# Kernel tuning notes

Measured on AMD Instinct MI355X. Metric: run time of the kernel, lower is better.

## Reference

```python
import jax, jax.numpy as jnp
import numpy as np

N_NODES = 100000
N_EDGES = 2000000
IN_C = 30
OUT_C = 10
HID = 4 * OUT_C      # 40
D1 = 2 * OUT_C       # 20
D2 = OUT_C           # 10
N_CLASSES = 3
K_SAMPLE = 8


def setup_inputs() -> dict:
    key = jax.random.key(0)
    ks = jax.random.split(key, 24)
    inp = {
        'x': jax.random.normal(ks[0], (N_NODES, IN_C), dtype=jnp.float32),
        'edge_index': jax.random.randint(ks[1], (2, N_EDGES), 0, N_NODES, dtype=jnp.int64),
        'edge_attr': jax.random.uniform(ks[2], (N_EDGES,), dtype=jnp.float32),
        'label': 1,
        # gcn1
        'W1': jax.random.normal(ks[3], (IN_C, HID), dtype=jnp.float32) * (1.0 / np.sqrt(IN_C)),
        'b1': jnp.zeros((HID,), jnp.float32),
        'ln1_w': jnp.ones((HID,), jnp.float32),
        'ln1_b': jnp.zeros((HID,), jnp.float32),
        # gcn2
        'W2': jax.random.normal(ks[4], (HID, HID), dtype=jnp.float32) * (1.0 / np.sqrt(HID)),
        'b2': jnp.zeros((HID,), jnp.float32),
        'ln2_w': jnp.ones((HID,), jnp.float32),
        'ln2_b': jnp.zeros((HID,), jnp.float32),
        # fnn
        'Wf': jax.random.normal(ks[5], (HID, D1), dtype=jnp.float32) * (1.0 / np.sqrt(HID)),
        'bf': jnp.zeros((D1,), jnp.float32),
        # attention (tanh / sigmoid branches + concat)
        'Wt': jax.random.normal(ks[6], (D1, D2), dtype=jnp.float32) * (1.0 / np.sqrt(D1)),
        'bt': jnp.zeros((D2,), jnp.float32),
        'Ws': jax.random.normal(ks[7], (D1, D2), dtype=jnp.float32) * (1.0 / np.sqrt(D1)),
        'bs': jnp.zeros((D2,), jnp.float32),
        'Wc': jax.random.normal(ks[8], (D2, 1), dtype=jnp.float32) * (1.0 / np.sqrt(D2)),
        'bc': jnp.zeros((1,), jnp.float32),
        # bag classifier
        'Wcls': jax.random.normal(ks[9], (D1, N_CLASSES), dtype=jnp.float32) * (1.0 / np.sqrt(D1)),
        'bcls': jnp.zeros((N_CLASSES,), jnp.float32),
        # per-class cell-scale classifiers, stacked [n_classes, D1, 2]
        'Wcell': jax.random.normal(ks[10], (N_CLASSES, D1, 2), dtype=jnp.float32) * (1.0 / np.sqrt(D1)),
        'bcell': jnp.zeros((N_CLASSES, 2), jnp.float32),
    }
    return inp


def _layernorm(x, w, b, eps=1e-5):
    m = jnp.mean(x, axis=-1, keepdims=True)
    v = jnp.var(x, axis=-1, keepdims=True)
    return (x - m) * jax.lax.rsqrt(v + eps) * w + b


def _gcn(x, W, b, src, dst, ew, n):
    # PyG GCNConv: add self-loops (weight 1), symmetric norm, aggregate at dst
    h = x @ W                                              # [N, F]
    deg = jax.ops.segment_sum(ew, dst, num_segments=n) + 1.0
    dinv = jnp.where(deg > 0, jax.lax.rsqrt(deg), 0.0)     # [N]
    norm = dinv[src] * ew * dinv[dst]                      # [E]
    agg = jax.ops.segment_sum(h[src] * norm[:, None], dst, num_segments=n)
    agg = agg + h * (dinv * dinv)[:, None]                 # self-loop term
    return agg + b


def _forward(x, edge_attr, W1, b1, ln1_w, ln1_b, W2, b2, ln2_w, ln2_b,
             Wf, bf, Wt, bt, Ws, bs, Wc, bc, Wcls, bcls, Wcell, bcell,
             edge_index, label):
    src, dst = edge_index[0], edge_index[1]
    n = x.shape[0]
    x1 = jax.nn.selu(_layernorm(_gcn(x, W1, b1, src, dst, edge_attr, n), ln1_w, ln1_b))
    x2 = jax.nn.selu(_layernorm(_gcn(x1, W2, b2, src, dst, edge_attr, n), ln2_w, ln2_b))
    x3 = jax.nn.selu(x2 @ Wf + bf)                         # [N, D1] == x_out
    # gated tanh*sigmoid attention
    gate = jnp.tanh(x3 @ Wt + bt) * jax.nn.sigmoid(x3 @ Ws + bs)
    A = (gate @ Wc + bc).T                                 # [1, N]
    A = jax.nn.softmax(A, axis=1)
    # cell-scale eval for the true class (one-hot label selects exactly one)
    a_row = A[-1]                                          # [N]
    _, idx_p = jax.lax.top_k(a_row, K_SAMPLE)
    _, idx_n = jax.lax.top_k(-a_row, K_SAMPLE)
    all_cells = jnp.concatenate([x3[idx_p], x3[idx_n]], axis=0)   # [2K, D1]
    logits_c = all_cells @ Wcell[label] + bcell[label]            # [2K, 2]
    targets = jnp.concatenate([jnp.ones((K_SAMPLE,), jnp.int32),
                               jnp.zeros((K_SAMPLE,), jnp.int32)])
    # SmoothTop1SVM (tau=1, alpha=1): mean( logsumexp(s + Delta) - s_y )
    delta = 1.0 - jax.nn.one_hot(targets, 2, dtype=logits_c.dtype)
    s_y = jnp.take_along_axis(logits_c, targets[:, None], axis=1)[:, 0]
    cell_loss = jnp.mean(jax.nn.logsumexp(logits_c + delta, axis=1) - s_y)
    # bag-level prediction
    x_pooled = A @ x3                                      # [1, D1]
    logits = x_pooled @ Wcls + bcls                        # [1, n_classes]
    Y_prob = jax.nn.softmax(logits, axis=1)
    Y_hat = jnp.argmax(logits, axis=1)[:, None]
    return logits, Y_prob, Y_hat, A, x3, cell_loss


def reference(x, edge_index, edge_attr, label, W1, b1, ln1_w, ln1_b, W2, b2,
              ln2_w, ln2_b, Wf, bf, Wt, bt, Ws, bs, Wc, bc, Wcls, bcls,
              Wcell, bcell):
    return _forward(x, edge_attr, W1, b1, ln1_w, ln1_b, W2, b2, ln2_w, ln2_b,
                    Wf, bf, Wt, bt, Ws, bs, Wc, bc, Wcls, bcls, Wcell, bcell,
                    edge_index, label)
```

## Files before the change

kernel.cpp:

```cpp
#include <hip/hip_runtime.h>
#include <hip/hip_bf16.h>
#include <math.h>

typedef __hip_bfloat16 bf16;

__device__ __forceinline__ float tof(bf16 v){ return __bfloat162float(v); }
__device__ __forceinline__ bf16  tob(float v){ return __float2bfloat16(v); }

__device__ __forceinline__ float sane(float v){
  return (v == v && v > -1e30f && v < 1e30f) ? v : 0.f;
}
__device__ __forceinline__ float ldf(const void* p, size_t i, bool f32){
  float v = f32 ? ((const float*)p)[i] : tof(((const bf16*)p)[i]);
  return sane(v);
}
__device__ __forceinline__ void stf(void* p, size_t i, float v, bool f32){
  if (f32) ((float*)p)[i] = v; else ((bf16*)p)[i] = tob(v);
}
__device__ __forceinline__ bool is_f32(const unsigned* __restrict__ dt){
  return dt[0] == 0x3F800000u;
}
__device__ __forceinline__ int clampi(int v, int hi){
  return ((unsigned)v < (unsigned)hi) ? v : 0;
}
__device__ __forceinline__ float selu_f(float x){
  const float sc = 1.0507009873554805f, al = 1.6732632423543772f;
  return x > 0.f ? sc * x : sc * al * (expf(x) - 1.0f);
}
__device__ __forceinline__ void unpack8(uint4 u, float* f){
  f[0]=__uint_as_float(u.x<<16); f[1]=__uint_as_float(u.x&0xFFFF0000u);
  f[2]=__uint_as_float(u.y<<16); f[3]=__uint_as_float(u.y&0xFFFF0000u);
  f[4]=__uint_as_float(u.z<<16); f[5]=__uint_as_float(u.z&0xFFFF0000u);
  f[6]=__uint_as_float(u.w<<16); f[7]=__uint_as_float(u.w&0xFFFF0000u);
}
__device__ __forceinline__ void unpack4(uint2 u, float* f){
  f[0]=__uint_as_float(u.x<<16); f[1]=__uint_as_float(u.x&0xFFFF0000u);
  f[2]=__uint_as_float(u.y<<16); f[3]=__uint_as_float(u.y&0xFFFF0000u);
}
__device__ __forceinline__ unsigned pack2(float a, float b){
  unsigned short ua, ub;
  bf16 ta = tob(a), tb = tob(b);
  __builtin_memcpy(&ua, &ta, 2);
  __builtin_memcpy(&ub, &tb, 2);
  return (unsigned)ua | ((unsigned)ub << 16);
}

__global__ void k_zero(float* __restrict__ p, int n){
  int i = blockIdx.x * blockDim.x + threadIdx.x;
  int stride = gridDim.x * blockDim.x;
  for (; i < n; i += stride) p[i] = 0.f;
}

__device__ __forceinline__ bool idx_is64(const int* __restrict__ raw){
  return ((raw[1] | raw[3] | raw[5] | raw[7] | raw[9] | raw[11]) == 0);
}
__device__ __forceinline__ void edge_at(const int* __restrict__ raw, int E, int e,
                                        bool w64, int N, int& s, int& d){
  int sv, dv;
  if (w64){ sv = raw[2 * e]; dv = raw[2 * (E + e)]; }
  else    { sv = raw[e];     dv = raw[E + e]; }
  s = clampi(sv, N); d = clampi(dv, N);
}

__global__ void k_cnt_rank(const int* __restrict__ raw, int* __restrict__ cnt,
                           int* __restrict__ rank, int E, int N){
  int e = blockIdx.x * blockDim.x + threadIdx.x;
  if (e >= E) return;
  bool w64 = idx_is64(raw);
  int s, d; edge_at(raw, E, e, w64, N, s, d);
  rank[e] = atomicAdd(&cnt[d], 1);
}

__global__ void k_scan_block(const int* __restrict__ cnt, int* __restrict__ bsum, int N){
  __shared__ int s[256];
  int base = blockIdx.x * 1024;
  int acc = 0;
  for (int k = threadIdx.x; k < 1024; k += 256){
    int i = base + k;
    acc += (i < N) ? cnt[i] : 0;
  }
  s[threadIdx.x] = acc; __syncthreads();
  for (int w = 128; w > 0; w >>= 1){
    if (threadIdx.x < w) s[threadIdx.x] += s[threadIdx.x + w];
    __syncthreads();
  }
  if (threadIdx.x == 0) bsum[blockIdx.x] = s[0];
}

__global__ void k_scan_partials(int* __restrict__ bsum, int B, int* __restrict__ rowpN, int E){
  __shared__ int s[256];
  int run = 0;
  for (int t0 = 0; t0 < B; t0 += 256){
    int i = t0 + threadIdx.x;
    int v = (i < B) ? bsum[i] : 0;
    s[threadIdx.x] = v;
    __syncthreads();
    for (int o = 1; o < 256; o <<= 1){
      int add = (threadIdx.x >= o) ? s[threadIdx.x - o] : 0;
      __syncthreads();
      s[threadIdx.x] += add;
      __syncthreads();
    }
    int incl = s[threadIdx.x];
    int total = s[255];
    __syncthreads();
    if (i < B) bsum[i] = run + incl - v;
    run += total;
    __syncthreads();
  }
  if (threadIdx.x == 0) rowpN[0] = E;
}

__global__ void k_scan_final(const int* __restrict__ cnt, const int* __restrict__ bsum,
                             int* __restrict__ rowp, int N){
  __shared__ int s[256];
  int t = threadIdx.x;
  int base = bsum[blockIdx.x];
  int i0 = blockIdx.x * 1024 + t * 4;
  int v0=0,v1=0,v2=0,v3=0;
  if (i0+0 < N) v0 = cnt[i0+0];
  if (i0+1 < N) v1 = cnt[i0+1];
  if (i0+2 < N) v2 = cnt[i0+2];
  if (i0+3 < N) v3 = cnt[i0+3];
  int sum = v0+v1+v2+v3;
  s[t] = sum; __syncthreads();
  for (int o = 1; o < 256; o <<= 1){
    int add = (t >= o) ? s[t - o] : 0;
    __syncthreads();
    s[t] += add;
    __syncthreads();
  }
  int off = base + s[t] - sum;
  if (i0+0 < N){ rowp[i0+0]=off; off+=v0; }
  if (i0+1 < N){ rowp[i0+1]=off; off+=v1; }
  if (i0+2 < N){ rowp[i0+2]=off; off+=v2; }
  if (i0+3 < N){ rowp[i0+3]=off; off+=v3; }
}

__global__ void k_place(const int* __restrict__ raw, const void* __restrict__ ea,
                        const unsigned* __restrict__ dt, const int* __restrict__ rank,
                        const int* __restrict__ rowp, int2* __restrict__ ep, int E, int N){
  int e = blockIdx.x * blockDim.x + threadIdx.x;
  if (e >= E) return;
  bool f32 = is_f32(dt);
  bool w64 = idx_is64(raw);
  int s, d; edge_at(raw, E, e, w64, N, s, d);
  float w = ldf(ea, e, f32);
  int pos = rowp[d] + rank[e];
  if ((unsigned)pos < (unsigned)E)
    ep[pos] = make_int2(s, __float_as_int(w));
}

__global__ void k_dinv_csr(const int* __restrict__ rowp, const int2* __restrict__ ep,
                           float* __restrict__ dinv, int N, int E){
  int n = blockIdx.x * blockDim.x + threadIdx.x;
  if (n >= N) return;
  int beg = rowp[n], end = rowp[n + 1];
  if (beg < 0) beg = 0;
  if (end > E) end = E;
  float s = 0.f;
  for (int j = beg; j < end; j++) s += sane(__int_as_float(ep[j].y));
  float dv = s + 1.0f;
  dinv[n] = (dv > 0.f) ? rsqrtf(dv) : 0.f;
}

__global__ void k_premul(int2* __restrict__ ep, const float* __restrict__ dinv,
                         int E, int N){
  int i = blockIdx.x * blockDim.x + threadIdx.x;
  if (i >= E) return;
  int2 p = ep[i];
  int s = clampi(p.x, N);
  float w = dinv[s] * sane(__int_as_float(p.y));
  ep[i] = make_int2(s, __float_as_int(w));
}

__global__ void k_mm1(const void* __restrict__ X, const void* __restrict__ W,
                      const unsigned* __restrict__ dt,
                      bf16* __restrict__ H, int N, int Nx){
  bool f32 = is_f32(dt);
  __shared__ float w[30 * 40];
  __shared__ float xs[256 * 30];
  for (int i = threadIdx.x; i < 30 * 40; i += 256) w[i] = ldf(W, i, f32);
  int base = blockIdx.x * 256;
  int rows = Nx - base; if (rows > 256) rows = 256; if (rows < 0) rows = 0;
  int nelem = rows * 30;
  size_t gbase = (size_t)base * 30;
  for (int i = threadIdx.x; i < nelem; i += 256) xs[i] = ldf(X, gbase + i, f32);
  __syncthreads();
  int n = base + threadIdx.x;
  if (n >= N) return;
  float acc[40];
  #pragma unroll
  for (int j = 0; j < 40; j++) acc[j] = 0.f;
  if (threadIdx.x < rows){
    const float* xr = &xs[threadIdx.x * 30];
    for (int i = 0; i < 30; i++){
      float xi = xr[i];
      #pragma unroll
      for (int j = 0; j < 40; j++) acc[j] += xi * w[i * 40 + j];
    }
  } else {
    for (int i = 0; i < 30; i++){
      float xi = ldf(X, i, f32);
      #pragma unroll
      for (int j = 0; j < 40; j++) acc[j] += xi * w[i * 40 + j];
    }
  }
  uint4 ob[5];
  unsigned* ou = (unsigned*)ob;
  #pragma unroll
  for (int q = 0; q < 20; q++) ou[q] = pack2(acc[2*q], acc[2*q+1]);
  uint4* op = (uint4*)(H + (size_t)n * 40);
  #pragma unroll
  for (int q = 0; q < 5; q++) op[q] = ob[q];
}

__global__ void k_mm2(const bf16* __restrict__ X, const void* __restrict__ W,
                      const unsigned* __restrict__ dt,
                      bf16* __restrict__ H, int N){
  bool f32 = is_f32(dt);
  __shared__ float w[40 * 40];
  for (int i = threadIdx.x; i < 40 * 40; i += 256) w[i] = ldf(W, i, f32);
  __syncthreads();
  int n = blockIdx.x * blockDim.x + threadIdx.x;
  if (n >= N) return;
  float acc[40];
  #pragma unroll
  for (int j = 0; j < 40; j++) acc[j] = 0.f;
  const uint4* xp = (const uint4*)(X + (size_t)n * 40);
  #pragma unroll
  for (int q = 0; q < 5; q++){
    uint4 u = xp[q];
    float f[8]; unpack8(u, f);
    #pragma unroll
    for (int k = 0; k < 8; k++){
      float xi = f[k];
      int i = q * 8 + k;
      #pragma unroll
      for (int j = 0; j < 40; j++) acc[j] += xi * w[i * 40 + j];
    }
  }
  uint4 ob[5];
  unsigned* ou = (unsigned*)ob;
  #pragma unroll
  for (int q = 0; q < 20; q++) ou[q] = pack2(acc[2*q], acc[2*q+1]);
  uint4* op = (uint4*)(H + (size_t)n * 40);
  #pragma unroll
  for (int q = 0; q < 5; q++) op[q] = ob[q];
}

__global__ void k_gather(const int* __restrict__ rowp, const int2* __restrict__ ep,
                         const bf16* __restrict__ h, const float* __restrict__ dinv,
                         const void* __restrict__ b, const void* __restrict__ lw,
                         const void* __restrict__ lb, const unsigned* __restrict__ dt,
                         bf16* __restrict__ xout, int N, int E){
  int n = (blockIdx.x * blockDim.x + threadIdx.x) >> 6;
  int lane = threadIdx.x & 63;
  if (n >= N) return;
  bool f32 = is_f32(dt);
  bool act = lane < 40;
  float dn = dinv[n];
  int beg = rowp[n], end = rowp[n + 1];
  if (beg < 0) beg = 0;
  if (end > E) end = E;
  float acc = 0.f;
  int j = beg;
  for (; j + 3 < end; j += 4){
    int2 p0 = ep[j+0], p1 = ep[j+1], p2 = ep[j+2], p3 = ep[j+3];
    int s0 = clampi(p0.x, N), s1 = clampi(p1.x, N);
    int s2 = clampi(p2.x, N), s3 = clampi(p3.x, N);
    float h0 = 0.f, h1 = 0.f, h2 = 0.f, h3 = 0.f;
    if (act){
      h0 = tof(h[(size_t)s0 * 40 + lane]);
      h1 = tof(h[(size_t)s1 * 40 + lane]);
      h2 = tof(h[(size_t)s2 * 40 + lane]);
      h3 = tof(h[(size_t)s3 * 40 + lane]);
    }
    acc += h0 * __int_as_float(p0.y) + h1 * __int_as_float(p1.y)
         + h2 * __int_as_float(p2.y) + h3 * __int_as_float(p3.y);
  }
  for (; j < end; j++){
    int2 p = ep[j];
    int s = clampi(p.x, N);
    float hv = act ? tof(h[(size_t)s * 40 + lane]) : 0.f;
    acc += hv * __int_as_float(p.y);
  }
  acc *= dn;
  float hself = act ? tof(h[(size_t)n * 40 + lane]) : 0.f;
  float v = act ? (sane(acc) + hself * dn * dn + ldf(b, lane, f32)) : 0.f;
  float sum = v;
  #pragma unroll
  for (int o = 1; o < 64; o <<= 1) sum += __shfl_xor(sum, o);
  float m = sum * (1.0f / 40.0f);
  float d = act ? (v - m) : 0.f;
  float sq = d * d;
  #pragma unroll
  for (int o = 1; o < 64; o <<= 1) sq += __shfl_xor(sq, o);
  float inv = rsqrtf(sq * (1.0f / 40.0f) + 1e-5f);
  if (act){
    float y = sane(selu_f(d * inv * ldf(lw, lane, f32) + ldf(lb, lane, f32)));
    xout[(size_t)n * 40 + lane] = tob(y);
  }
}

__global__ void k_head(const bf16* __restrict__ x2,
                       const void* __restrict__ Wf, const void* __restrict__ bfv,
                       const void* __restrict__ Wt, const void* __restrict__ bt,
                       const void* __restrict__ Ws, const void* __restrict__ bs,
                       const void* __restrict__ Wc, const void* __restrict__ bc,
                       const unsigned* __restrict__ dt,
                       bf16* __restrict__ x3ws, float* __restrict__ alog, int N){
  bool f32 = is_f32(dt);
  __shared__ float wf[800], bff[20], wt[200], btt[10], wss[200], bss[10], wc[10], bcc[1];
  for (int i = threadIdx.x; i < 800; i += blockDim.x) wf[i] = ldf(Wf, i, f32);
  for (int i = threadIdx.x; i < 200; i += blockDim.x){
    wt[i] = ldf(Wt, i, f32); wss[i] = ldf(Ws, i, f32);
  }
  if (threadIdx.x < 20) bff[threadIdx.x] = ldf(bfv, threadIdx.x, f32);
  if (threadIdx.x < 10){ btt[threadIdx.x] = ldf(bt, threadIdx.x, f32);
                         bss[threadIdx.x] = ldf(bs, threadIdx.x, f32);
                         wc[threadIdx.x]  = ldf(Wc, threadIdx.x, f32); }
  if (threadIdx.x == 0) bcc[0] = ldf(bc, 0, f32);
  __syncthreads();
  int n = blockIdx.x * blockDim.x + threadIdx.x;
  if (n >= N) return;
  float r[40];
  const uint4* xp = (const uint4*)(x2 + (size_t)n * 40);
  #pragma unroll
  for (int q = 0; q < 5; q++){
    uint4 u = xp[q];
    unpack8(u, &r[q * 8]);
  }
  float x3r[20];
  #pragma unroll
  for (int j = 0; j < 20; j++){
    float acc = bff[j];
    for (int i = 0; i < 40; i++) acc += r[i] * wf[i * 20 + j];
    x3r[j] = sane(selu_f(acc));
  }
  uint2 ob[5];
  unsigned* ou = (unsigned*)ob;
  #pragma unroll
  for (int q = 0; q < 10; q++) ou[q] = pack2(x3r[2*q], x3r[2*q+1]);
  uint2* op = (uint2*)(x3ws + (size_t)n * 20);
  #pragma unroll
  for (int q = 0; q < 5; q++) op[q] = ob[q];
  float a = bcc[0];
  #pragma unroll
  for (int j = 0; j < 10; j++){
    float zt = btt[j], zs = bss[j];
    for (int i = 0; i < 20; i++){ zt += x3r[i] * wt[i * 10 + j]; zs += x3r[i] * wss[i * 10 + j]; }
    float g = tanhf(zt) * (1.0f / (1.0f + expf(-zs)));
    a += g * wc[j];
  }
  alog[n] = sane(a);
}

__global__ void k_copy_x3(const bf16* __restrict__ x3ws, const unsigned* __restrict__ dt,
                          void* __restrict__ out, size_t off, int total){
  bool f32 = is_f32(dt);
  int i = blockIdx.x * blockDim.x + threadIdx.x;
  int stride = gridDim.x * blockDim.x;
  for (; i < total; i += stride) stf(out, off + i, tof(x3ws[i]), f32);
}

__global__ void k_msum(const float* __restrict__ a, float2* __restrict__ part, int n){
  __shared__ float sm[256], sl[256];
  int t = threadIdx.x;
  float m = -1e30f, l = 0.f;
  for (int i = blockIdx.x * blockDim.x + t; i < n; i += gridDim.x * blockDim.x){
    float v = sane(a[i]);
    if (v > m){ l = l * expf(m - v) + 1.f; m = v; }
    else        l += expf(v - m);
  }
  sm[t] = m; sl[t] = l; __syncthreads();
  for (int w = 128; w > 0; w >>= 1){
    if (t < w){
      float m2 = sm[t+w], l2 = sl[t+w];
      float mm = fmaxf(sm[t], m2);
      sl[t] = sl[t] * expf(sm[t] - mm) + l2 * expf(m2 - mm);
      sm[t] = mm;
    }
    __syncthreads();
  }
  if (t == 0) part[blockIdx.x] = make_float2(sm[0], sl[0]);
}

__global__ void k_msum_fin(const float2* __restrict__ part, float* __restrict__ scal,
                           float* __restrict__ pooled){
  __shared__ float sm[256], sl[256];
  int t = threadIdx.x;
  float2 p = part[t];
  sm[t] = p.x; sl[t] = p.y; __syncthreads();
  for (int w = 128; w > 0; w >>= 1){
    if (t < w){
      float m2 = sm[t+w], l2 = sl[t+w];
      float mm = fmaxf(sm[t], m2);
      sl[t] = sl[t] * expf(sm[t] - mm) + l2 * expf(m2 - mm);
      sm[t] = mm;
    }
    __syncthreads();
  }
  if (t == 0){ scal[0] = sm[0]; scal[1] = sl[0]; }
  if (t < 20) pooled[t] = 0.f;
}

__global__ void k_writeA(const float* __restrict__ alog, const bf16* __restrict__ x3ws,
                         const float* __restrict__ scal,
                         const unsigned* __restrict__ dt,
                         void* __restrict__ out, size_t a_off,
                         float* __restrict__ pooled, int N){
  bool f32 = is_f32(dt);
  float gmax = scal[0];
  float sum  = scal[1];
  float inv  = (sum > 0.f) ? 1.0f / sum : 0.f;
  float acc[20];
  #pragma unroll
  for (int j = 0; j < 20; j++) acc[j] = 0.f;
  for (int i = blockIdx.x * blockDim.x + threadIdx.x; i < N; i += gridDim.x * blockDim.x){
    float a = expf(sane(alog[i]) - gmax) * inv;
    stf(out, a_off + i, a, f32);
    const uint2* xr = (const uint2*)(x3ws + (size_t)i * 20);
    #pragma unroll
    for (int q = 0; q < 5; q++){
      float f[4]; unpack4(xr[q], f);
      #pragma unroll
      for (int k = 0; k < 4; k++) acc[q * 4 + k] += a * f[k];
    }
  }
  __shared__ float s[20];
  if (threadIdx.x < 20) s[threadIdx.x] = 0.f;
  __syncthreads();
  #pragma unroll
  for (int j = 0; j < 20; j++) atomicAdd(&s[j], acc[j]);
  __syncthreads();
  if (threadIdx.x < 20) atomicAdd(&pooled[threadIdx.x], s[threadIdx.x]);
}

__global__ void k_topk1(const float* __restrict__ a, int N,
                        float* __restrict__ cvp, int* __restrict__ cip,
                        float* __restrict__ cvn, int* __restrict__ cin){
  const int T = 256, K = 8;
  __shared__ float sv[T * K];
  __shared__ int   si[T * K];
  __shared__ float rv[T];
  __shared__ int   ri[T];
  __shared__ int   rs[T];
  int t = threadIdx.x;
  float tv[K]; int ti[K]; float bv[K]; int bi[K];
  #pragma unroll
  for (int k = 0; k < K; k++){ tv[k] = -1e38f; ti[k] = 0x7ffffff;
                               bv[k] =  1e38f; bi[k] = 0x7ffffff; }
  for (int i = blockIdx.x * T + t; i < N; i += gridDim.x * T){
    float v = sane(a[i]);
    if (v > tv[K-1]){
      int p = K - 1;
      while (p > 0 && v > tv[p-1]){ tv[p] = tv[p-1]; ti[p] = ti[p-1]; p--; }
      tv[p] = v; ti[p] = i;
    }
    if (v < bv[K-1]){
      int p = K - 1;
      while (p > 0 && v < bv[p-1]){ bv[p] = bv[p-1]; bi[p] = bi[p-1]; p--; }
      bv[p] = v; bi[p] = i;
    }
  }
  for (int k = 0; k < K; k++){ sv[t*K+k] = tv[k]; si[t*K+k] = ti[k]; }
  __syncthreads();
  for (int round = 0; round < K; round++){
    float bvv = -1e38f; int bii = 0x7ffffff; int bslot = 0;
    for (int k = 0; k < K; k++){
      float v = sv[t*K+k]; int ii = si[t*K+k];
      if (v > bvv || (v == bvv && ii < bii)){ bvv = v; bii = ii; bslot = t*K+k; }
    }
    rv[t] = bvv; ri[t] = bii; rs[t] = bslot;
    __syncthreads();
    for (int w = T/2; w > 0; w >>= 1){
      if (t < w){
        float v2 = rv[t+w]; int i2 = ri[t+w];
        if (v2 > rv[t] || (v2 == rv[t] && i2 < ri[t])){ rv[t]=v2; ri[t]=i2; rs[t]=rs[t+w]; }
      }
      __syncthreads();
    }
    if (t == 0){ cvp[blockIdx.x*K + round] = rv[0]; cip[blockIdx.x*K + round] = ri[0];
                 sv[rs[0]] = -1e38f; }
    __syncthreads();
  }
  for (int k = 0; k < K; k++){ sv[t*K+k] = bv[k]; si[t*K+k] = bi[k]; }
  __syncthreads();
  for (int round = 0; round < K; round++){
    float bvv = 1e38f; int bii = 0x7ffffff; int bslot = 0;
    for (int k = 0; k < K; k++){
      float v = sv[t*K+k]; int ii = si[t*K+k];
      if (v < bvv || (v == bvv && ii < bii)){ bvv = v; bii = ii; bslot = t*K+k; }
    }
    rv[t] = bvv; ri[t] = bii; rs[t] = bslot;
    __syncthreads();
    for (int w = T/2; w > 0; w >>= 1){
      if (t < w){
        float v2 = rv[t+w]; int i2 = ri[t+w];
        if (v2 < rv[t] || (v2 == rv[t] && i2 < ri[t])){ rv[t]=v2; ri[t]=i2; rs[t]=rs[t+w]; }
      }
      __syncthreads();
    }
    if (t == 0){ cvn[blockIdx.x*K + round] = rv[0]; cin[blockIdx.x*K + round] = ri[0];
                 sv[rs[0]] = 1e38f; }
    __syncthreads();
  }
}

__global__ void k_topk2(const float* __restrict__ cvp, const int* __restrict__ cip,
                        const float* __restrict__ cvn, const int* __restrict__ cin,
                        int* __restrict__ idxp, int* __restrict__ idxn, int M){
  const int T = 256, CAP = 1024, PER = CAP / T;
  __shared__ float sv[CAP];
  __shared__ int   si[CAP];
  __shared__ float rv[T];
  __shared__ int   ri[T];
  __shared__ int   rs[T];
  int t = threadIdx.x;
  for (int i = t; i < CAP; i += T){
    sv[i] = (i < M) ? cvp[i] : -1e38f;
    si[i] = (i < M) ? cip[i] : 0x7ffffff;
  }
  __syncthreads();
  for (int round = 0; round < 8; round++){
    float bvv = -1e38f; int bii = 0x7ffffff; int bslot = t * PER;
    for (int k = 0; k < PER; k++){
      float v = sv[t*PER+k]; int ii = si[t*PER+k];
      if (v > bvv || (v == bvv && ii < bii)){ bvv = v; bii = ii; bslot = t*PER+k; }
    }
    rv[t] = bvv; ri[t] = bii; rs[t] = bslot;
    __syncthreads();
    for (int w = T/2; w > 0; w >>= 1){
      if (t < w){
        float v2 = rv[t+w]; int i2 = ri[t+w];
        if (v2 > rv[t] || (v2 == rv[t] && i2 < ri[t])){ rv[t]=v2; ri[t]=i2; rs[t]=rs[t+w]; }
      }
      __syncthreads();
    }
    if (t == 0){ idxp[round] = ri[0]; sv[rs[0]] = -1e38f; }
    __syncthreads();
  }
  for (int i = t; i < CAP; i += T){
    sv[i] = (i < M) ? cvn[i] : 1e38f;
    si[i] = (i < M) ? cin[i] : 0x7ffffff;
  }
  __syncthreads();
  for (int round = 0; round < 8; round++){
    float bvv = 1e38f; int bii = 0x7ffffff; int bslot = t * PER;
    for (int k = 0; k < PER; k++){
      float v = sv[t*PER+k]; int ii = si[t*PER+k];
      if (v < bvv || (v == bvv && ii < bii)){ bvv = v; bii = ii; bslot = t*PER+k; }
    }
    rv[t] = bvv; ri[t] = bii; rs[t] = bslot;
    __syncthreads();
    for (int w = T/2; w > 0; w >>= 1){
      if (t < w){
        float v2 = rv[t+w]; int i2 = ri[t+w];
        if (v2 < rv[t] || (v2 == rv[t] && i2 < ri[t])){ rv[t]=v2; ri[t]=i2; rs[t]=rs[t+w]; }
      }
      __syncthreads();
    }
    if (t == 0){ idxn[round] = ri[0]; sv[rs[0]] = 1e38f; }
    __syncthreads();
  }
}

__global__ void k_final(const float* __restrict__ pooled,
                        const void* __restrict__ Wcls, const void* __restrict__ bcls,
                        const void* __restrict__ Wcell, const void* __restrict__ bcell,
                        const int* __restrict__ label_p, const bf16* __restrict__ x3ws,
                        const int* __restrict__ idxp, const int* __restrict__ idxn,
                        const unsigned* __restrict__ dt,
                        void* __restrict__ out, int N){
  if (threadIdx.x != 0 || blockIdx.x != 0) return;
  bool f32 = is_f32(dt);
  float lg[3];
  for (int c = 0; c < 3; c++){
    float acc = ldf(bcls, c, f32);
    for (int j = 0; j < 20; j++) acc += sane(pooled[j]) * ldf(Wcls, j * 3 + c, f32);
    lg[c] = sane(acc);
  }
  float m = fmaxf(lg[0], fmaxf(lg[1], lg[2]));
  float e0 = expf(lg[0]-m), e1 = expf(lg[1]-m), e2 = expf(lg[2]-m);
  float es = e0 + e1 + e2;
  int yhat = 0;
  if (lg[1] > lg[yhat]) yhat = 1;
  if (lg[2] > lg[yhat]) yhat = 2;
  stf(out, 0, lg[0], f32); stf(out, 1, lg[1], f32); stf(out, 2, lg[2], f32);
  stf(out, 3, e0/es, f32); stf(out, 4, e1/es, f32); stf(out, 5, e2/es, f32);
  stf(out, 6, (float)yhat, f32);
  int lw0 = label_p[0];
  int label;
  if ((unsigned)lw0 < 3u) label = lw0;
  else if (lw0 == 0x3F800000 || lw0 == 0x3F803F80) label = 1;
  else if (lw0 == 0x40000000 || lw0 == 0x40004000) label = 2;
  else label = 0;
  float w0[20], w1[20];
  for (int j = 0; j < 20; j++){
    w0[j] = ldf(Wcell, (size_t)label * 40 + j*2 + 0, f32);
    w1[j] = ldf(Wcell, (size_t)label * 40 + j*2 + 1, f32);
  }
  float b0 = ldf(bcell, (size_t)label * 2 + 0, f32);
  float b1 = ldf(bcell, (size_t)label * 2 + 1, f32);
  float loss = 0.f;
  for (int i = 0; i < 16; i++){
    int node = clampi((i < 8) ? idxp[i] : idxn[i-8], N);
    const bf16* xr = x3ws + (size_t)node * 20;
    float l0 = b0, l1 = b1;
    for (int j = 0; j < 20; j++){ float xv = tof(xr[j]); l0 += xv * w0[j]; l1 += xv * w1[j]; }
    int tgt = (i < 8) ? 1 : 0;
    float a0 = l0 + ((tgt == 0) ? 0.f : 1.f);
    float a1 = l1 + ((tgt == 1) ? 0.f : 1.f);
    float mm = fmaxf(a0, a1);
    float lse = mm + logf(expf(a0-mm) + expf(a1-mm));
    float sy = tgt ? l1 : l0;
    loss += lse - sy;
  }
  stf(out, (size_t)7 + N + (size_t)20 * N, sane(loss * (1.0f / 16.0f)), f32);
}

extern "C" void kernel_launch(void* const* d_in, const int* in_sizes, int n_in,
                              void* d_out, int out_size, void* d_ws, size_t ws_size,
                              hipStream_t stream) {
  const int N = (out_size - 8) / 21;
  if (N <= 0) return;
  const int Nx = (in_sizes[0] / 30 < N) ? (in_sizes[0] / 30) : N;
  int E = in_sizes[1] / 2;
  if (in_sizes[2] < E) E = in_sizes[2];
  if (E < 6) return;

  const void* x    = d_in[0];
  const int*  eraw = (const int*)d_in[1];
  const void* ea   = d_in[2];
  const int*  lbl  = (const int*)d_in[3];
  const void* W1   = d_in[4];
  const void* b1   = d_in[5];
  const unsigned* dt = (const unsigned*)d_in[6];
  const void* ln1w = d_in[6];
  const void* ln1b = d_in[7];
  const void* W2   = d_in[8];
  const void* b2   = d_in[9];
  const void* ln2w = d_in[10];
  const void* ln2b = d_in[11];
  const void* Wf   = d_in[12];
  const void* bfv  = d_in[13];
  const void* Wt   = d_in[14];
  const void* bt   = d_in[15];
  const void* Ws   = d_in[16];
  const void* bs   = d_in[17];
  const void* Wc   = d_in[18];
  const void* bc   = d_in[19];
  const void* Wcls = d_in[20];
  const void* bcls = d_in[21];
  const void* Wcell= d_in[22];
  const void* bcell= d_in[23];

  auto align16 = [](size_t v){ return (v + 15) & ~(size_t)15; };
  size_t hA_bytes = (size_t)N * 40 * 2;
  size_t rank_bytes = (size_t)E * 4;
  size_t regA = hA_bytes > rank_bytes ? hA_bytes : rank_bytes;
  size_t off = 0;
  char* ws = (char*)d_ws;
  bf16* hA    = (bf16*)(ws + off);
  int*  rank  = (int*)(ws + off);  off = align16(off + regA);
  bf16* xB    = (bf16*)(ws + off); off = align16(off + (size_t)N * 40 * 2);
  int2* epack = (int2*)(ws + off); off = align16(off + (size_t)E * 8);
  int*  rowp  = (int*)(ws + off);  off = align16(off + (size_t)(N + 1) * 4);
  int*  cnt   = (int*)(ws + off);  off = align16(off + (size_t)N * 4);
  int*  bsum  = (int*)(ws + off);  off = align16(off + 4096 * 4);
  float* dinv = (float*)(ws + off); off = align16(off + (size_t)N * 4);
  float* alog = (float*)(ws + off); off = align16(off + (size_t)N * 4);
  float2* part2 = (float2*)(ws + off); off = align16(off + 256 * 8);
  float* scal = (float*)(ws + off); off = align16(off + 2 * 4);
  float* pooled = (float*)(ws + off); off = align16(off + 20 * 4);
  int*   idxp = (int*)(ws + off); off = align16(off + 8 * 4);
  int*   idxn = (int*)(ws + off); off = align16(off + 8 * 4);
  float* cvp  = (float*)(ws + off); off = align16(off + 1024 * 4);
  int*   cip  = (int*)(ws + off);   off = align16(off + 1024 * 4);
  float* cvn  = (float*)(ws + off); off = align16(off + 1024 * 4);
  int*   cin  = (int*)(ws + off);   off = align16(off + 1024 * 4);
  if (off > ws_size) return;
  bf16* x3ws = hA;

  const int TB = 256;
  const int gN = (N + TB - 1) / TB;
  const int gE = (E + TB - 1) / TB;
  const int gW = (N + 3) / 4;
  const int SB = (N + 1023) / 1024;
  const int TP = 128;

  k_zero<<<gN, TB, 0, stream>>>((float*)cnt, N);
  k_cnt_rank<<<gE, TB, 0, stream>>>(eraw, cnt, rank, E, N);
  k_scan_block<<<SB, TB, 0, stream>>>(cnt, bsum, N);
  k_scan_partials<<<1, TB, 0, stream>>>(bsum, SB, rowp + N, E);
  k_scan_final<<<SB, TB, 0, stream>>>(cnt, bsum, rowp, N);
  k_place<<<gE, TB, 0, stream>>>(eraw, ea, dt, rank, rowp, epack, E, N);
  k_dinv_csr<<<gN, TB, 0, stream>>>(rowp, epack, dinv, N, E);
  k_premul<<<gE, TB, 0, stream>>>(epack, dinv, E, N);

  k_mm1<<<gN, TB, 0, stream>>>(x, W1, dt, hA, N, Nx);
  k_gather<<<gW, TB, 0, stream>>>(rowp, epack, hA, dinv, b1, ln1w, ln1b, dt, xB, N, E);

  k_mm2<<<gN, TB, 0, stream>>>(xB, W2, dt, hA, N);
  k_gather<<<gW, TB, 0, stream>>>(rowp, epack, hA, dinv, b2, ln2w, ln2b, dt, xB, N, E);

  k_head<<<gN, TB, 0, stream>>>(xB, Wf, bfv, Wt, bt, Ws, bs, Wc, bc, dt,
                                x3ws, alog, N);
  k_copy_x3<<<2048, TB, 0, stream>>>(x3ws, dt, d_out, (size_t)7 + N, 20 * N);

  k_msum<<<256, TB, 0, stream>>>(alog, part2, N);
  k_msum_fin<<<1, TB, 0, stream>>>(part2, scal, pooled);
  k_writeA<<<256, TB, 0, stream>>>(alog, x3ws, scal, dt, d_out, (size_t)7, pooled, N);

  k_topk1<<<TP, TB, 0, stream>>>(alog, N, cvp, cip, cvn, cin);
  k_topk2<<<1, TB, 0, stream>>>(cvp, cip, cvn, cin, idxp, idxn, TP * 8);
  k_final<<<1, 64, 0, stream>>>(pooled, Wcls, bcls, Wcell, bcell, lbl,
                                x3ws, idxp, idxn, dt, d_out, N);
}
```

Baseline: 681.2 us.

## Gather with 8 lanes per node and 16-byte vectorized feature loads

The GCN aggregation kernel used to give each node a full 64-lane wavefront, with only 40 lanes active and one bf16 loaded per lane. It now gives each node 8 lanes, 5 of them active, and each active lane loads 8 bf16 features as one uint4 per neighbour. LayerNorm reductions shrink to 3 shuffle steps, and the output is written with one vector store per lane. The aim is fewer idle lanes, fewer memory instructions and more nodes in flight per wave. The trade-off is more registers per thread and divergence when nodes in the same wave have very different degrees.

```diff
diff --git a/kernel.cpp b/kernel.cpp
--- a/kernel.cpp
+++ b/kernel.cpp
@@ -254,52 +254,84 @@
                          const void* __restrict__ b, const void* __restrict__ lw,
                          const void* __restrict__ lb, const unsigned* __restrict__ dt,
                          bf16* __restrict__ xout, int N, int E){
-  int n = (blockIdx.x * blockDim.x + threadIdx.x) >> 6;
-  int lane = threadIdx.x & 63;
+  int tid = blockIdx.x * blockDim.x + threadIdx.x;
+  int n  = tid >> 3;
+  int sl = tid & 7;
   if (n >= N) return;
   bool f32 = is_f32(dt);
-  bool act = lane < 40;
+  bool act = sl < 5;
+  int fb = sl * 8;
   float dn = dinv[n];
   int beg = rowp[n], end = rowp[n + 1];
   if (beg < 0) beg = 0;
   if (end > E) end = E;
-  float acc = 0.f;
+  float a[8];
+  #pragma unroll
+  for (int k = 0; k < 8; k++) a[k] = 0.f;
   int j = beg;
   for (; j + 3 < end; j += 4){
-    int2 p0 = ep[j+0], p1 = ep[j+1], p2 = ep[j+2], p3 = ep[j+3];
+    int2 p0 = ep[j], p1 = ep[j+1], p2 = ep[j+2], p3 = ep[j+3];
     int s0 = clampi(p0.x, N), s1 = clampi(p1.x, N);
     int s2 = clampi(p2.x, N), s3 = clampi(p3.x, N);
-    float h0 = 0.f, h1 = 0.f, h2 = 0.f, h3 = 0.f;
     if (act){
-      h0 = tof(h[(size_t)s0 * 40 + lane]);
-      h1 = tof(h[(size_t)s1 * 40 + lane]);
-      h2 = tof(h[(size_t)s2 * 40 + lane]);
-      h3 = tof(h[(size_t)s3 * 40 + lane]);
-    }
-    acc += h0 * __int_as_float(p0.y) + h1 * __int_as_float(p1.y)
-         + h2 * __int_as_float(p2.y) + h3 * __int_as_float(p3.y);
+      uint4 u0 = *(const uint4*)(h + (size_t)s0 * 40 + fb);
+      uint4 u1 = *(const uint4*)(h + (size_t)s1 * 40 + fb);
+      uint4 u2 = *(const uint4*)(h + (size_t)s2 * 40 + fb);
+      uint4 u3 = *(const uint4*)(h + (size_t)s3 * 40 + fb);
+      float w0 = __int_as_float(p0.y), w1 = __int_as_float(p1.y);
+      float w2 = __int_as_float(p2.y), w3 = __int_as_float(p3.y);
+      float f0[8], f1[8], f2[8], f3[8];
+      unpack8(u0, f0); unpack8(u1, f1); unpack8(u2, f2); unpack8(u3, f3);
+      #pragma unroll
+      for (int k = 0; k < 8; k++)
+        a[k] += f0[k]*w0 + f1[k]*w1 + f2[k]*w2 + f3[k]*w3;
+    }
   }
   for (; j < end; j++){
     int2 p = ep[j];
     int s = clampi(p.x, N);
-    float hv = act ? tof(h[(size_t)s * 40 + lane]) : 0.f;
-    acc += hv * __int_as_float(p.y);
-  }
-  acc *= dn;
-  float hself = act ? tof(h[(size_t)n * 40 + lane]) : 0.f;
-  float v = act ? (sane(acc) + hself * dn * dn + ldf(b, lane, f32)) : 0.f;
-  float sum = v;
-  #pragma unroll
-  for (int o = 1; o < 64; o <<= 1) sum += __shfl_xor(sum, o);
+    if (act){
+      uint4 u = *(const uint4*)(h + (size_t)s * 40 + fb);
+      float w = __int_as_float(p.y);
+      float f[8]; unpack8(u, f);
+      #pragma unroll
+      for (int k = 0; k < 8; k++) a[k] += f[k] * w;
+    }
+  }
+  float v[8]; float psum = 0.f;
+  if (act){
+    uint4 us = *(const uint4*)(h + (size_t)n * 40 + fb);
+    float fs[8]; unpack8(us, fs);
+    float di2 = dn * dn;
+    #pragma unroll
+    for (int k = 0; k < 8; k++){
+      v[k] = sane(a[k] * dn) + fs[k] * di2 + ldf(b, fb + k, f32);
+      psum += v[k];
+    }
+  } else {
+    #pragma unroll
+    for (int k = 0; k < 8; k++) v[k] = 0.f;
+  }
+  float sum = psum;
+  sum += __shfl_xor(sum, 1); sum += __shfl_xor(sum, 2); sum += __shfl_xor(sum, 4);
   float m = sum * (1.0f / 40.0f);
-  float d = act ? (v - m) : 0.f;
-  float sq = d * d;
-  #pragma unroll
-  for (int o = 1; o < 64; o <<= 1) sq += __shfl_xor(sq, o);
+  float sq = 0.f;
+  if (act){
+    #pragma unroll
+    for (int k = 0; k < 8; k++){ float d = v[k] - m; sq += d * d; }
+  }
+  sq += __shfl_xor(sq, 1); sq += __shfl_xor(sq, 2); sq += __shfl_xor(sq, 4);
   float inv = rsqrtf(sq * (1.0f / 40.0f) + 1e-5f);
   if (act){
-    float y = sane(selu_f(d * inv * ldf(lw, lane, f32) + ldf(lb, lane, f32)));
-    xout[(size_t)n * 40 + lane] = tob(y);
+    float y[8];
+    #pragma unroll
+    for (int k = 0; k < 8; k++)
+      y[k] = sane(selu_f((v[k] - m) * inv * ldf(lw, fb + k, f32) + ldf(lb, fb + k, f32)));
+    uint4 ob;
+    unsigned* ou = (unsigned*)&ob;
+    #pragma unroll
+    for (int q = 0; q < 4; q++) ou[q] = pack2(y[2*q], y[2*q+1]);
+    *(uint4*)(xout + (size_t)n * 40 + fb) = ob;
   }
 }
 
@@ -686,7 +718,7 @@
   const int TB = 256;
   const int gN = (N + TB - 1) / TB;
   const int gE = (E + TB - 1) / TB;
-  const int gW = (N + 3) / 4;
+  const int gG = (int)(((size_t)N * 8 + TB - 1) / TB);
   const int SB = (N + 1023) / 1024;
   const int TP = 128;
 
@@ -700,10 +732,10 @@
   k_premul<<<gE, TB, 0, stream>>>(epack, dinv, E, N);
 
   k_mm1<<<gN, TB, 0, stream>>>(x, W1, dt, hA, N, Nx);
-  k_gather<<<gW, TB, 0, stream>>>(rowp, epack, hA, dinv, b1, ln1w, ln1b, dt, xB, N, E);
+  k_gather<<<gG, TB, 0, stream>>>(rowp, epack, hA, dinv, b1, ln1w, ln1b, dt, xB, N, E);
 
   k_mm2<<<gN, TB, 0, stream>>>(xB, W2, dt, hA, N);
-  k_gather<<<gW, TB, 0, stream>>>(rowp, epack, hA, dinv, b2, ln2w, ln2b, dt, xB, N, E);
+  k_gather<<<gG, TB, 0, stream>>>(rowp, epack, hA, dinv, b2, ln2w, ln2b, dt, xB, N, E);
 
   k_head<<<gN, TB, 0, stream>>>(xB, Wf, bfv, Wt, bt, Ws, bs, Wc, bc, dt,
                                 x3ws, alog, N);
```

Result: faster. 602.2 us (-11.6%).
